# Performance work log

Measured on AMD Instinct MI355X. Metric: run time of the kernel, lower is better.

Reference implementation:

```python
import jax, jax.numpy as jnp
import numpy as np

DEGREE = 5
LN_EPS = 1e-5


def _xavier(key, shape):
    fan_in, fan_out = shape[-1] if len(shape) == 2 else shape[1] * shape[2], shape[0]
    limit = float(np.sqrt(6.0 / (fan_in + fan_out)))
    return jax.random.uniform(key, shape, jnp.float32, -limit, limit)


def setup_inputs() -> dict:
    key = jax.random.key(0)
    ks = jax.random.split(key, 6)
    B, D0, D1, D2 = 16384, 1024, 1024, 512
    return {
        "x": jax.random.normal(ks[0], (B, D0), jnp.float32),
        "coeff1": _xavier(ks[1], (D1, D0, DEGREE + 1)),
        "base_w1": _xavier(ks[2], (D1, D0)),
        "bias1": jnp.zeros((D1,), jnp.float32),
        "ln_gamma": jnp.ones((D1,), jnp.float32),
        "ln_beta": jnp.zeros((D1,), jnp.float32),
        "coeff2": _xavier(ks[3], (D2, D1, DEGREE + 1)),
        "base_w2": _xavier(ks[4], (D2, D1)),
        "bias2": jnp.zeros((D2,), jnp.float32),
    }


def _cheb_layer(x, coeff, base_w, bias):
    # x: [B, I]; coeff: [O, I, D+1]; base_w: [O, I]; bias: [O]
    xn = jnp.tanh(x)
    polys = [jnp.ones_like(xn), xn]
    for _ in range(2, DEGREE + 1):
        polys.append(2.0 * xn * polys[-1] - polys[-2])
    cheb = jnp.stack(polys, axis=-1)  # [B, I, D+1]
    y = jnp.einsum("bid,oid->bo", cheb, coeff)
    y = y + x @ base_w.T + bias
    return y


def _layernorm(h, gamma, beta):
    mu = jnp.mean(h, axis=-1, keepdims=True)
    var = jnp.mean(jnp.square(h - mu), axis=-1, keepdims=True)
    return (h - mu) * jax.lax.rsqrt(var + LN_EPS) * gamma + beta


def reference(x, coeff1, base_w1, bias1, ln_gamma, ln_beta, coeff2, base_w2, bias2):
    x = jnp.tanh(x)  # input_normalization='tanh'
    h = _cheb_layer(x, coeff1, base_w1, bias1)
    h = _layernorm(h, ln_gamma, ln_beta)
    h = h * jax.nn.sigmoid(h)  # SiLU
    out = _cheb_layer(h, coeff2, base_w2, bias2)
    return out
```

## Files before the change

### kernel.cpp

```cpp
#include <hip/hip_runtime.h>


typedef __bf16 bf16x8 __attribute__((ext_vector_type(8)));
typedef float f32x4 __attribute__((ext_vector_type(4)));
typedef unsigned short u16x8 __attribute__((ext_vector_type(8)));

__device__ __forceinline__ unsigned short f2bf(float f) {
    unsigned int u = __float_as_uint(f);
    unsigned int r = (u + 0x7FFFu + ((u >> 16) & 1u)) >> 16;
    return (unsigned short)r;
}
__device__ __forceinline__ float bf2f(unsigned short b) {
    return __uint_as_float(((unsigned int)b) << 16);
}

__device__ __forceinline__ float fast_tanh(float x) {
    float a = fminf(fmaxf(x, -15.f), 15.f);
    float e = __expf(2.f * a);
    return 1.f - 2.f * __builtin_amdgcn_rcpf(e + 1.f);
}
__device__ __forceinline__ float fast_silu(float y) {
    float a = fminf(fmaxf(y, -30.f), 30.f);
    return y * __builtin_amdgcn_rcpf(1.f + __expf(-a));
}

__device__ __forceinline__ void cheb_pack(float s, unsigned short* o6) {
    float u  = fast_tanh(s);
    float T1 = u;
    float T2 = 2.f * u * u - 1.f;
    float T3 = 2.f * u * T2 - T1;
    float T4 = 2.f * u * T3 - T2;
    float T5 = 2.f * u * T4 - T3;
    o6[0] = f2bf(T1); o6[1] = f2bf(T2); o6[2] = f2bf(T3);
    o6[3] = f2bf(T4); o6[4] = f2bf(T5); o6[5] = f2bf(s);
}

__device__ __forceinline__ void load_lds16(const void* g, void* l) {
    __builtin_amdgcn_global_load_lds(
        (const __attribute__((address_space(1))) void*)g,
        (__attribute__((address_space(3))) void*)l, 16, 0, 0);
}

__global__ __launch_bounds__(256) void prep_w_kernel(
    const float* __restrict__ coeff, const float* __restrict__ base_w,
    unsigned short* __restrict__ W, int OI)
{
    int idx = blockIdx.x * 256 + threadIdx.x;
    if (idx >= OI) return;
    const float* c = coeff + (size_t)idx * 6;
    unsigned short w0 = f2bf(c[1]), w1 = f2bf(c[2]), w2 = f2bf(c[3]),
                   w3 = f2bf(c[4]), w4 = f2bf(c[5]), w5 = f2bf(base_w[idx]);
    unsigned int* d = (unsigned int*)(W + (size_t)idx * 6);
    d[0] = w0 | ((unsigned int)w1 << 16);
    d[1] = w2 | ((unsigned int)w3 << 16);
    d[2] = w4 | ((unsigned int)w5 << 16);
}

__global__ __launch_bounds__(256) void prep_bias_kernel(
    const float* __restrict__ coeff, const float* __restrict__ bias,
    float* __restrict__ bp, int I)
{
    int o = blockIdx.x, tid = threadIdx.x;
    float s = 0.f;
    for (int i = tid; i < I; i += 256) s += coeff[((size_t)o * I + i) * 6];
    #pragma unroll
    for (int off = 32; off > 0; off >>= 1) s += __shfl_down(s, off);
    __shared__ float red[4];
    int lane = tid & 63, wv = tid >> 6;
    if (lane == 0) red[wv] = s;
    __syncthreads();
    if (tid == 0) bp[o] = bias[o] + red[0] + red[1] + red[2] + red[3];
}

__global__ __launch_bounds__(256) void expand1_kernel(
    const float* __restrict__ x, unsigned short* __restrict__ Xa)
{
    int b = blockIdx.x, tid = threadIdx.x;
    f32x4 xv = *(const f32x4*)(x + (size_t)b * 1024 + tid * 4);
    alignas(16) unsigned short ov[24];
    #pragma unroll
    for (int e = 0; e < 4; e++) cheb_pack(fast_tanh(xv[e]), ov + e * 6);
    u16x8* dst = (u16x8*)(Xa + (size_t)b * 6144 + tid * 24);
    const u16x8* src = (const u16x8*)ov;
    dst[0] = src[0]; dst[1] = src[1]; dst[2] = src[2];
}

__global__ __launch_bounds__(256) void ln_silu_expand_kernel(
    const unsigned short* __restrict__ H, const float* __restrict__ gamma,
    const float* __restrict__ beta, unsigned short* __restrict__ Xa)
{
    int b = blockIdx.x, tid = threadIdx.x;
    ushort4 hb = *(const ushort4*)(H + (size_t)b * 1024 + tid * 4);
    float hv[4] = { bf2f(hb.x), bf2f(hb.y), bf2f(hb.z), bf2f(hb.w) };
    float s1 = hv[0] + hv[1] + hv[2] + hv[3];
    float s2 = hv[0]*hv[0] + hv[1]*hv[1] + hv[2]*hv[2] + hv[3]*hv[3];
    #pragma unroll
    for (int off = 32; off > 0; off >>= 1) {
        s1 += __shfl_down(s1, off);
        s2 += __shfl_down(s2, off);
    }
    __shared__ float red[8];
    __shared__ float stats[2];
    int lane = tid & 63, wv = tid >> 6;
    if (lane == 0) { red[wv] = s1; red[4 + wv] = s2; }
    __syncthreads();
    if (tid == 0) {
        float t1 = red[0] + red[1] + red[2] + red[3];
        float t2 = red[4] + red[5] + red[6] + red[7];
        float mu = t1 * (1.f / 1024.f);
        float var = t2 * (1.f / 1024.f) - mu * mu;
        stats[0] = mu;
        stats[1] = rsqrtf(var + 1e-5f);
    }
    __syncthreads();
    float mu = stats[0], rs = stats[1];
    f32x4 g  = *(const f32x4*)(gamma + tid * 4);
    f32x4 bt = *(const f32x4*)(beta  + tid * 4);
    alignas(16) unsigned short ov[24];
    #pragma unroll
    for (int e = 0; e < 4; e++) {
        float y = (hv[e] - mu) * rs * g[e] + bt[e];
        cheb_pack(fast_silu(y), ov + e * 6);
    }
    u16x8* dst = (u16x8*)(Xa + (size_t)b * 6144 + tid * 24);
    const u16x8* src = (const u16x8*)ov;
    dst[0] = src[0]; dst[1] = src[1]; dst[2] = src[2];
}

template<int BM, bool OUT_BF16>
__global__ __launch_bounds__(256, 4) void gemm_kernel(
    const unsigned short* __restrict__ A,
    const unsigned short* __restrict__ Wt,
    const float* __restrict__ bias,
    void* __restrict__ Cout,
    int N, int K)
{
    constexpr int MI = BM / 32;
    __shared__ __align__(16) unsigned short As[BM * 64];
    __shared__ __align__(16) unsigned short Bs[128 * 64];
    const int tid  = threadIdx.x;
    const int lane = tid & 63;
    const int wave = tid >> 6;
    const int ntn  = N >> 7;

    int bkid = blockIdx.x;
    const int nm = gridDim.x / ntn;
    int mt, nt;
    if ((nm & 7) == 0) {
        const int mg = nm >> 3;
        const int s  = bkid >> 3;
        const int q  = s / ntn;
        mt = (bkid & 7) * mg + q;
        nt = s - q * ntn;
    } else {
        mt = bkid / ntn; nt = bkid % ntn;
    }
    const size_t m0 = (size_t)mt * BM;
    const size_t n0 = (size_t)nt << 7;

    const int wr = (wave >> 1) * (BM / 2);
    const int wc = (wave & 1) * 64;
    const int fr = lane & 15;
    const int cg = lane >> 4;
    const int srow = tid >> 3;
    const int schunk = (tid & 7) ^ (srow & 7);

    const int fr7 = fr & 7;
    const unsigned short* fA0 = As + (wr + fr) * 64 + ((cg    ) ^ fr7) * 8;
    const unsigned short* fA1 = As + (wr + fr) * 64 + ((cg + 4) ^ fr7) * 8;
    const unsigned short* fB0 = Bs + (wc + fr) * 64 + ((cg    ) ^ fr7) * 8;
    const unsigned short* fB1 = Bs + (wc + fr) * 64 + ((cg + 4) ^ fr7) * 8;

    const unsigned short* Agu = A  + m0 * (size_t)K;
    const unsigned short* Bgu = Wt + n0 * (size_t)K;
    const int loff = srow * K + schunk * 8;

    f32x4 acc[MI][4];
    #pragma unroll
    for (int i = 0; i < MI; i++)
        #pragma unroll
        for (int j = 0; j < 4; j++) acc[i][j] = f32x4{0.f, 0.f, 0.f, 0.f};

    for (int k0 = 0; k0 < K; k0 += 64) {
        const unsigned short* ak = Agu + k0;
        const unsigned short* bk = Bgu + k0;
        #pragma unroll
        for (int s = 0; s < BM / 32; ++s)
            load_lds16(ak + s * 32 * K + loff, &As[(s * 256 + wave * 64) * 8]);
        #pragma unroll
        for (int s = 0; s < 4; ++s)
            load_lds16(bk + s * 32 * K + loff, &Bs[(s * 256 + wave * 64) * 8]);
        __syncthreads();

        bf16x8 af[MI], bfr[4];
        #pragma unroll
        for (int i = 0; i < MI; i++) af[i]  = *(const bf16x8*)(fA0 + i * 1024);
        #pragma unroll
        for (int j = 0; j < 4; j++)  bfr[j] = *(const bf16x8*)(fB0 + j * 1024);
        #pragma unroll
        for (int i = 0; i < MI; i++)
            #pragma unroll
            for (int j = 0; j < 4; j++)
                acc[i][j] = __builtin_amdgcn_mfma_f32_16x16x32_bf16(
                    af[i], bfr[j], acc[i][j], 0, 0, 0);
        #pragma unroll
        for (int i = 0; i < MI; i++) af[i]  = *(const bf16x8*)(fA1 + i * 1024);
        #pragma unroll
        for (int j = 0; j < 4; j++)  bfr[j] = *(const bf16x8*)(fB1 + j * 1024);
        #pragma unroll
        for (int i = 0; i < MI; i++)
            #pragma unroll
            for (int j = 0; j < 4; j++)
                acc[i][j] = __builtin_amdgcn_mfma_f32_16x16x32_bf16(
                    af[i], bfr[j], acc[i][j], 0, 0, 0);
        __syncthreads();
    }

    const int rbase = wr + (lane >> 4) * 4;
    const int cbase = wc + (lane & 15);
    #pragma unroll
    for (int j = 0; j < 4; j++) {
        const int col = (int)n0 + cbase + j * 16;
        const float bv = bias[col];
        #pragma unroll
        for (int i = 0; i < MI; i++) {
            #pragma unroll
            for (int r = 0; r < 4; r++) {
                const size_t idx = (m0 + rbase + i * 16 + r) * N + col;
                if (OUT_BF16)
                    ((unsigned short*)Cout)[idx] = f2bf(acc[i][j][r] + bv);
                else
                    ((float*)Cout)[idx] = acc[i][j][r] + bv;
            }
        }
    }
}

extern "C" void kernel_launch(void* const* d_in, const int* in_sizes, int n_in,
                              void* d_out, int out_size, void* d_ws, size_t ws_size,
                              hipStream_t stream)
{
    const float* x       = (const float*)d_in[0];
    const float* coeff1  = (const float*)d_in[1];
    const float* base_w1 = (const float*)d_in[2];
    const float* bias1   = (const float*)d_in[3];
    const float* gamma   = (const float*)d_in[4];
    const float* beta    = (const float*)d_in[5];
    const float* coeff2  = (const float*)d_in[6];
    const float* base_w2 = (const float*)d_in[7];
    const float* bias2   = (const float*)d_in[8];
    float* out = (float*)d_out;

    const int B = 16384, D0 = 1024, D1 = 1024, D2 = 512;
    const int K1 = D0 * 6, K2 = D1 * 6;

    char* base = (char*)d_ws;
    size_t off = 0;
    unsigned short* W1 = (unsigned short*)(base + off); off += (size_t)D1 * K1 * 2;
    unsigned short* W2 = (unsigned short*)(base + off); off += (size_t)D2 * K2 * 2;
    float* b1p = (float*)(base + off); off += (size_t)D1 * 4;
    float* b2p = (float*)(base + off); off += (size_t)D2 * 4;
    off = (off + 255) & ~(size_t)255;

    size_t per_row = (size_t)K1 * 2 + (size_t)D1 * 2;
    long long avail = (long long)ws_size - (long long)off;
    long long mcl = avail > 0 ? avail / (long long)per_row : 0;
    int Mc = (int)((mcl / 128) * 128);
    if (Mc < 128) Mc = 128;
    if (Mc > B) Mc = B;

    unsigned short* Xa = (unsigned short*)(base + off);
    unsigned short* h = (unsigned short*)(base + off + (size_t)Mc * K1 * 2);

    prep_w_kernel<<<(D1 * D0 + 255) / 256, 256, 0, stream>>>(coeff1, base_w1, W1, D1 * D0);
    prep_w_kernel<<<(D2 * D1 + 255) / 256, 256, 0, stream>>>(coeff2, base_w2, W2, D2 * D1);
    prep_bias_kernel<<<D1, 256, 0, stream>>>(coeff1, bias1, b1p, D0);
    prep_bias_kernel<<<D2, 256, 0, stream>>>(coeff2, bias2, b2p, D1);

    for (int m0 = 0; m0 < B; m0 += Mc) {
        int rows = (B - m0 < Mc) ? (B - m0) : Mc;
        expand1_kernel<<<rows, 256, 0, stream>>>(x + (size_t)m0 * D0, Xa);
        gemm_kernel<128, true><<<(rows / 128) * (D1 / 128), 256, 0, stream>>>(
            Xa, W1, b1p, h, D1, K1);
        ln_silu_expand_kernel<<<rows, 256, 0, stream>>>(h, gamma, beta, Xa);
        gemm_kernel<64, false><<<(rows / 64) * (D2 / 128), 256, 0, stream>>>(
            Xa, W2, b2p, out + (size_t)m0 * D2, D2, K2);
    }
}
```

Before: 627.2 us.

## Replace GEMM with 8-wave 256-row tile, double-buffered LDS ping-pong pipeline

Replaces the single-buffered 4-wave GEMM with an 8-wave kernel that uses 256-row tiles, 256- or 128-column tiles and double-buffered LDS. Global-to-LDS loads for the next K tiles are interleaved between MFMA phases, with explicit vmcnt waits, barriers and s_setprio. The goal is to hide memory latency behind compute and raise arithmetic intensity per tile. The costs are much more LDS per block, lower occupancy (launch bounds of 2 blocks per CU), and a chunk size that must now be a multiple of 256 rows.

```diff
diff --git a/kernel.cpp b/kernel.cpp
--- a/kernel.cpp
+++ b/kernel.cpp
@@ -127,113 +127,191 @@
     dst[0] = src[0]; dst[1] = src[1]; dst[2] = src[2];
 }
 
-template<int BM, bool OUT_BF16>
-__global__ __launch_bounds__(256, 4) void gemm_kernel(
+#define FENCE() asm volatile("" ::: "memory")
+
+#define PH_MID() do { \
+    FENCE(); __builtin_amdgcn_s_barrier(); \
+    asm volatile("s_waitcnt lgkmcnt(0)" ::: "memory"); \
+    __builtin_amdgcn_sched_barrier(0); \
+    __builtin_amdgcn_s_setprio(1); } while (0)
+
+#define PH_END() do { \
+    __builtin_amdgcn_s_setprio(0); \
+    FENCE(); __builtin_amdgcn_s_barrier(); FENCE(); } while (0)
+
+#define VM_STEADY() do { \
+    if constexpr (BN == 256) asm volatile("s_waitcnt vmcnt(8)" ::: "memory"); \
+    else                     asm volatile("s_waitcnt vmcnt(6)" ::: "memory"); } while (0)
+#define VM_DRAIN() asm volatile("s_waitcnt vmcnt(0)" ::: "memory")
+
+#define RD_A(DST0, DST1, BASE, MH) do { \
+    _Pragma("unroll") \
+    for (int mf = 0; mf < 4; ++mf) { \
+        const unsigned short* p_ = (BASE) + ((MH) * 64 + mf * 16) * 64; \
+        DST0[mf] = *(const bf16x8*)(p_ + c0); \
+        DST1[mf] = *(const bf16x8*)(p_ + c1); \
+    } } while (0)
+
+#define RD_B(DST, BASE, CSEL) do { \
+    _Pragma("unroll") \
+    for (int nf = 0; nf < FN; ++nf) \
+        DST[nf] = *(const bf16x8*)((BASE) + (nf * 16) * 64 + (CSEL)); \
+    } while (0)
+
+#define QUAD(MH, AV, BV) do { \
+    _Pragma("unroll") \
+    for (int mf = 0; mf < 4; ++mf) \
+        _Pragma("unroll") \
+        for (int nf = 0; nf < FN; ++nf) \
+            acc[MH][mf][nf] = __builtin_amdgcn_mfma_f32_16x16x32_bf16( \
+                AV[mf], BV[nf], acc[MH][mf][nf], 0, 0, 0); \
+    } while (0)
+
+template<int BN, bool OUT_BF16>
+__global__ __launch_bounds__(512, 2) void gemm8_kernel(
     const unsigned short* __restrict__ A,
     const unsigned short* __restrict__ Wt,
     const float* __restrict__ bias,
     void* __restrict__ Cout,
-    int N, int K)
-{
-    constexpr int MI = BM / 32;
-    __shared__ __align__(16) unsigned short As[BM * 64];
-    __shared__ __align__(16) unsigned short Bs[128 * 64];
+    int N, int K, int NMT)
+{
+    constexpr int FN   = BN / 64;
+    constexpr int BUPW = BN / 64;
+
+    __shared__ __align__(16) unsigned short As[2 * 256 * 64];
+    __shared__ __align__(16) unsigned short Bs[2 * BN * 64];
+
     const int tid  = threadIdx.x;
     const int lane = tid & 63;
     const int wave = tid >> 6;
-    const int ntn  = N >> 7;
-
-    int bkid = blockIdx.x;
-    const int nm = gridDim.x / ntn;
-    int mt, nt;
-    if ((nm & 7) == 0) {
-        const int mg = nm >> 3;
-        const int s  = bkid >> 3;
-        const int q  = s / ntn;
-        mt = (bkid & 7) * mg + q;
-        nt = s - q * ntn;
-    } else {
-        mt = bkid / ntn; nt = bkid % ntn;
-    }
-    const size_t m0 = (size_t)mt * BM;
-    const size_t n0 = (size_t)nt << 7;
-
-    const int wr = (wave >> 1) * (BM / 2);
-    const int wc = (wave & 1) * 64;
-    const int fr = lane & 15;
-    const int cg = lane >> 4;
-    const int srow = tid >> 3;
-    const int schunk = (tid & 7) ^ (srow & 7);
-
+    const int wm   = wave >> 2;
+    const int wn   = wave & 3;
+
+    int wg = blockIdx.x;
+    {
+        const int nwg = gridDim.x;
+        if ((nwg & 7) == 0) {
+            const int cpx = nwg >> 3;
+            wg = (wg & 7) * cpx + (wg >> 3);
+        }
+    }
+    const int mt = wg % NMT;
+    const int nt = wg / NMT;
+    const size_t m0 = (size_t)mt * 256;
+    const size_t n0 = (size_t)nt * BN;
+
+    const int srow   = lane >> 3;
+    const int schunk = (lane & 7) ^ (srow & 7);
+    const unsigned short* Ag = A  + (m0 + srow) * (size_t)K + schunk * 8;
+    const unsigned short* Bg = Wt + (n0 + srow) * (size_t)K + schunk * 8;
+
+    const int fr  = lane & 15;
+    const int cg  = lane >> 4;
     const int fr7 = fr & 7;
-    const unsigned short* fA0 = As + (wr + fr) * 64 + ((cg    ) ^ fr7) * 8;
-    const unsigned short* fA1 = As + (wr + fr) * 64 + ((cg + 4) ^ fr7) * 8;
-    const unsigned short* fB0 = Bs + (wc + fr) * 64 + ((cg    ) ^ fr7) * 8;
-    const unsigned short* fB1 = Bs + (wc + fr) * 64 + ((cg + 4) ^ fr7) * 8;
-
-    const unsigned short* Agu = A  + m0 * (size_t)K;
-    const unsigned short* Bgu = Wt + n0 * (size_t)K;
-    const int loff = srow * K + schunk * 8;
-
-    f32x4 acc[MI][4];
-    #pragma unroll
-    for (int i = 0; i < MI; i++)
+    const int c0  = ((cg    ) ^ fr7) << 3;
+    const int c1  = ((cg + 4) ^ fr7) << 3;
+
+    const int NT = K >> 6;
+
+    const unsigned short* A0f = As + fr * 64 + (wm * 128) * 64;
+    const unsigned short* A1f = A0f + 256 * 64;
+    const unsigned short* B0f = Bs + fr * 64 + (wn * (BN / 4)) * 64;
+    const unsigned short* B1f = B0f + BN * 64;
+
+    auto stageA = [&](int kt, int bsel) {
+        const unsigned short* g = Ag + kt * 64;
+        unsigned short* l = As + bsel * (256 * 64);
         #pragma unroll
-        for (int j = 0; j < 4; j++) acc[i][j] = f32x4{0.f, 0.f, 0.f, 0.f};
-
-    for (int k0 = 0; k0 < K; k0 += 64) {
-        const unsigned short* ak = Agu + k0;
-        const unsigned short* bk = Bgu + k0;
+        for (int j = 0; j < 4; ++j) {
+            const int u = wave * 4 + j;
+            load_lds16(g + (size_t)(u * 8) * K, l + u * 512);
+        }
+    };
+    auto stageB = [&](int kt, int bsel) {
+        const unsigned short* g = Bg + kt * 64;
+        unsigned short* l = Bs + bsel * (BN * 64);
         #pragma unroll
-        for (int s = 0; s < BM / 32; ++s)
-            load_lds16(ak + s * 32 * K + loff, &As[(s * 256 + wave * 64) * 8]);
+        for (int j = 0; j < BUPW; ++j) {
+            const int u = wave * BUPW + j;
+            load_lds16(g + (size_t)(u * 8) * K, l + u * 512);
+        }
+    };
+
+    f32x4 acc[2][4][FN];
+    #pragma unroll
+    for (int mh = 0; mh < 2; ++mh)
         #pragma unroll
-        for (int s = 0; s < 4; ++s)
-            load_lds16(bk + s * 32 * K + loff, &Bs[(s * 256 + wave * 64) * 8]);
-        __syncthreads();
-
-        bf16x8 af[MI], bfr[4];
+        for (int mf = 0; mf < 4; ++mf)
+            #pragma unroll
+            for (int nf = 0; nf < FN; ++nf)
+                acc[mh][mf][nf] = f32x4{0.f, 0.f, 0.f, 0.f};
+
+    stageB(0, 0); stageA(0, 0);
+    stageB(1, 1); stageA(1, 1);
+    VM_STEADY();
+    FENCE(); __builtin_amdgcn_s_barrier(); FENCE();
+
+    for (int kt = 0; kt < NT; kt += 2) {
+        const bool st = (kt + 4) <= NT;
+        bf16x8 a0[4], a1[4], b0[FN], b1[FN];
+
+        RD_A(a0, a1, A0f, 0);
+        RD_B(b0, B0f, c0);
+        PH_MID(); QUAD(0, a0, b0); PH_END();
+
+        RD_B(b1, B0f, c1);
+        PH_MID(); QUAD(0, a1, b1); PH_END();
+
+        RD_A(a0, a1, A0f, 1);
+        if (st) stageB(kt + 2, 0);
+        PH_MID(); QUAD(1, a0, b0); PH_END();
+
+        if (st) { stageA(kt + 2, 0); VM_STEADY(); }
+        else    { VM_DRAIN(); }
+        PH_MID(); QUAD(1, a1, b1); PH_END();
+
+        RD_A(a0, a1, A1f, 0);
+        RD_B(b0, B1f, c0);
+        PH_MID(); QUAD(0, a0, b0); PH_END();
+
+        RD_B(b1, B1f, c1);
+        PH_MID(); QUAD(0, a1, b1); PH_END();
+
+        RD_A(a0, a1, A1f, 1);
+        if (st) stageB(kt + 3, 1);
+        PH_MID(); QUAD(1, a0, b0); PH_END();
+
+        if (st) { stageA(kt + 3, 1); VM_STEADY(); }
+        else    { VM_DRAIN(); }
+        PH_MID(); QUAD(1, a1, b1); PH_END();
+    }
+
+    const size_t rbase0 = m0 + wm * 128 + ((lane >> 4) << 2);
+    const int cb = lane & 15;
+    int colg[FN]; float bv[FN];
+    #pragma unroll
+    for (int nf = 0; nf < FN; ++nf) {
+        colg[nf] = (int)n0 + wn * (BN / 4) + nf * 16 + cb;
+        bv[nf] = bias[colg[nf]];
+    }
+    #pragma unroll
+    for (int mh = 0; mh < 2; ++mh)
         #pragma unroll
-        for (int i = 0; i < MI; i++) af[i]  = *(const bf16x8*)(fA0 + i * 1024);
-        #pragma unroll
-        for (int j = 0; j < 4; j++)  bfr[j] = *(const bf16x8*)(fB0 + j * 1024);
-        #pragma unroll
-        for (int i = 0; i < MI; i++)
+        for (int mf = 0; mf < 4; ++mf) {
+            const size_t rg0 = rbase0 + mh * 64 + mf * 16;
             #pragma unroll
-            for (int j = 0; j < 4; j++)
-                acc[i][j] = __builtin_amdgcn_mfma_f32_16x16x32_bf16(
-                    af[i], bfr[j], acc[i][j], 0, 0, 0);
-        #pragma unroll
-        for (int i = 0; i < MI; i++) af[i]  = *(const bf16x8*)(fA1 + i * 1024);
-        #pragma unroll
-        for (int j = 0; j < 4; j++)  bfr[j] = *(const bf16x8*)(fB1 + j * 1024);
-        #pragma unroll
-        for (int i = 0; i < MI; i++)
-            #pragma unroll
-            for (int j = 0; j < 4; j++)
-                acc[i][j] = __builtin_amdgcn_mfma_f32_16x16x32_bf16(
-                    af[i], bfr[j], acc[i][j], 0, 0, 0);
-        __syncthreads();
-    }
-
-    const int rbase = wr + (lane >> 4) * 4;
-    const int cbase = wc + (lane & 15);
-    #pragma unroll
-    for (int j = 0; j < 4; j++) {
-        const int col = (int)n0 + cbase + j * 16;
-        const float bv = bias[col];
-        #pragma unroll
-        for (int i = 0; i < MI; i++) {
-            #pragma unroll
-            for (int r = 0; r < 4; r++) {
-                const size_t idx = (m0 + rbase + i * 16 + r) * N + col;
-                if (OUT_BF16)
-                    ((unsigned short*)Cout)[idx] = f2bf(acc[i][j][r] + bv);
-                else
-                    ((float*)Cout)[idx] = acc[i][j][r] + bv;
+            for (int r = 0; r < 4; ++r) {
+                const size_t rowoff = (rg0 + r) * (size_t)N;
+                #pragma unroll
+                for (int nf = 0; nf < FN; ++nf) {
+                    const float v = acc[mh][mf][nf][r] + bv[nf];
+                    if constexpr (OUT_BF16)
+                        ((unsigned short*)Cout)[rowoff + colg[nf]] = f2bf(v);
+                    else
+                        ((float*)Cout)[rowoff + colg[nf]] = v;
+                }
             }
         }
-    }
 }
 
 extern "C" void kernel_launch(void* const* d_in, const int* in_sizes, int n_in,
@@ -265,8 +343,8 @@
     size_t per_row = (size_t)K1 * 2 + (size_t)D1 * 2;
     long long avail = (long long)ws_size - (long long)off;
     long long mcl = avail > 0 ? avail / (long long)per_row : 0;
-    int Mc = (int)((mcl / 128) * 128);
-    if (Mc < 128) Mc = 128;
+    int Mc = (int)((mcl / 256) * 256);
+    if (Mc < 256) Mc = 256;
     if (Mc > B) Mc = B;
 
     unsigned short* Xa = (unsigned short*)(base + off);
@@ -279,11 +357,12 @@
 
     for (int m0 = 0; m0 < B; m0 += Mc) {
         int rows = (B - m0 < Mc) ? (B - m0) : Mc;
+        int nmt = rows / 256;
         expand1_kernel<<<rows, 256, 0, stream>>>(x + (size_t)m0 * D0, Xa);
-        gemm_kernel<128, true><<<(rows / 128) * (D1 / 128), 256, 0, stream>>>(
-            Xa, W1, b1p, h, D1, K1);
+        gemm8_kernel<256, true><<<nmt * (D1 / 256), 512, 0, stream>>>(
+            Xa, W1, b1p, h, D1, K1, nmt);
         ln_silu_expand_kernel<<<rows, 256, 0, stream>>>(h, gamma, beta, Xa);
-        gemm_kernel<64, false><<<(rows / 64) * (D2 / 128), 256, 0, stream>>>(
-            Xa, W2, b2p, out + (size_t)m0 * D2, D2, K2);
-    }
-}
+        gemm8_kernel<128, false><<<nmt * (D2 / 128), 512, 0, stream>>>(
+            Xa, W2, b2p, out + (size_t)m0 * D2, D2, K2, nmt);
+    }
+}
```

Result: slower. 678.8 us (+8.2%).

## Add 256x256 eight-wave double-buffered GEMM for first Chebyshev layer

Applied to the files above, without the earlier changes.

Replaces the first-layer GEMM with a new 512-thread kernel that computes 256x256 output tiles. It double-buffers A and B in LDS with direct global-to-LDS loads and uses hand-placed waitcnt, barrier and setprio calls to overlap MFMA work with LDS reads and global prefetch. The larger tile is meant to raise arithmetic intensity and hide memory latency. In exchange it uses far more LDS (128 KB) and registers per block, so occupancy is lower, and the row chunk size is now rounded to 256.

```diff
diff --git a/kernel.cpp b/kernel.cpp
--- a/kernel.cpp
+++ b/kernel.cpp
@@ -127,14 +127,207 @@
     dst[0] = src[0]; dst[1] = src[1]; dst[2] = src[2];
 }
 
-template<int BM, bool OUT_BF16>
+#define FENCE() asm volatile("" ::: "memory")
+#define MIDB()  do { FENCE(); __builtin_amdgcn_s_barrier(); } while (0)
+#define ENDB()  do { __builtin_amdgcn_s_setprio(0); FENCE(); \
+                     __builtin_amdgcn_s_barrier(); FENCE(); } while (0)
+#define LG0() do { asm volatile("s_waitcnt lgkmcnt(0)" ::: "memory"); \
+                   __builtin_amdgcn_sched_barrier(0); } while (0)
+#define LG4() do { asm volatile("s_waitcnt lgkmcnt(4)" ::: "memory"); \
+                   __builtin_amdgcn_sched_barrier(0); } while (0)
+#define LG8() do { asm volatile("s_waitcnt lgkmcnt(8)" ::: "memory"); \
+                   __builtin_amdgcn_sched_barrier(0); } while (0)
+#define VMC0() asm volatile("s_waitcnt vmcnt(0)" ::: "memory")
+#define VMC4() asm volatile("s_waitcnt vmcnt(4)" ::: "memory")
+#define VMC8() asm volatile("s_waitcnt vmcnt(8)" ::: "memory")
+#define SB0()  __builtin_amdgcn_sched_barrier(0)
+
+#define RD_A4(DST, BASE, MH, CS) do { \
+    _Pragma("unroll") \
+    for (int mf = 0; mf < 4; ++mf) \
+        DST[mf] = *(const bf16x8*)((BASE) + ((MH) * 64 + mf * 16) * 64 + (CS)); \
+    } while (0)
+#define RD_B4(DST, BASE, CS) do { \
+    _Pragma("unroll") \
+    for (int nf = 0; nf < 4; ++nf) \
+        DST[nf] = *(const bf16x8*)((BASE) + (nf * 16) * 64 + (CS)); \
+    } while (0)
+
+#define QUAD(MH, AV, BV) do { \
+    __builtin_amdgcn_s_setprio(1); \
+    _Pragma("unroll") \
+    for (int mf = 0; mf < 4; ++mf) \
+        _Pragma("unroll") \
+        for (int nf = 0; nf < 4; ++nf) \
+            acc[MH][mf][nf] = __builtin_amdgcn_mfma_f32_16x16x32_bf16( \
+                AV[mf], BV[nf], acc[MH][mf][nf], 0, 0, 0); \
+    } while (0)
+
+__global__ __launch_bounds__(512, 2) void gemm8_kernel(
+    const unsigned short* __restrict__ A,
+    const unsigned short* __restrict__ Wt,
+    const float* __restrict__ bias,
+    unsigned short* __restrict__ Cout,
+    int N, int K, int NMT)
+{
+    __shared__ __align__(16) unsigned short As[2 * 256 * 64];
+    __shared__ __align__(16) unsigned short Bs[2 * 256 * 64];
+
+    const int tid  = threadIdx.x;
+    const int lane = tid & 63;
+    const int wave = tid >> 6;
+    const int wm   = wave >> 2;
+    const int wn   = wave & 3;
+
+    int wg = blockIdx.x;
+    {
+        const int nwg = gridDim.x;
+        if ((nwg & 7) == 0) {
+            const int cpx = nwg >> 3;
+            wg = (wg & 7) * cpx + (wg >> 3);
+        }
+    }
+    const int mt = wg % NMT;
+    const int nt = wg / NMT;
+    const size_t m0 = (size_t)mt * 256;
+    const size_t n0 = (size_t)nt * 256;
+
+    const int srow   = lane >> 3;
+    const int schunk = (lane & 7) ^ (srow & 7);
+    const unsigned short* Ag = A  + (m0 + srow) * (size_t)K + schunk * 8;
+    const unsigned short* Bg = Wt + (n0 + srow) * (size_t)K + schunk * 8;
+
+    const int fr  = lane & 15;
+    const int cg  = lane >> 4;
+    const int fr7 = fr & 7;
+    const int c0  = ((cg    ) ^ fr7) << 3;
+    const int c1  = ((cg + 4) ^ fr7) << 3;
+
+    const int NT = K >> 6;
+
+    const unsigned short* A0f = As + fr * 64 + (wm * 128) * 64;
+    const unsigned short* A1f = A0f + 256 * 64;
+    const unsigned short* B0f = Bs + fr * 64 + (wn * 64) * 64;
+    const unsigned short* B1f = B0f + 256 * 64;
+
+    auto stageA = [&](int kt, int bsel) {
+        const unsigned short* g = Ag + kt * 64;
+        unsigned short* l = As + bsel * (256 * 64);
+        #pragma unroll
+        for (int j = 0; j < 4; ++j) {
+            const int u = wave * 4 + j;
+            load_lds16(g + (size_t)(u * 8) * K, l + u * 512);
+        }
+    };
+    auto stageB = [&](int kt, int bsel) {
+        const unsigned short* g = Bg + kt * 64;
+        unsigned short* l = Bs + bsel * (256 * 64);
+        #pragma unroll
+        for (int j = 0; j < 4; ++j) {
+            const int u = wave * 4 + j;
+            load_lds16(g + (size_t)(u * 8) * K, l + u * 512);
+        }
+    };
+
+    f32x4 acc[2][4][4];
+    #pragma unroll
+    for (int mh = 0; mh < 2; ++mh)
+        #pragma unroll
+        for (int mf = 0; mf < 4; ++mf)
+            #pragma unroll
+            for (int nf = 0; nf < 4; ++nf)
+                acc[mh][mf][nf] = f32x4{0.f, 0.f, 0.f, 0.f};
+
+    bf16x8 aP[4], aQ[4], b0[4], b1[4];
+
+    stageB(0, 0); stageA(0, 0); stageB(1, 1);
+    VMC4();
+    MIDB(); FENCE();
+    RD_B4(b0, B0f, c0);
+    SB0();
+
+    for (int kt = 0; kt < NT; kt += 2) {
+        const bool st = (kt + 4) <= NT;
+
+        RD_A4(aP, A0f, 0, c0);
+        SB0();
+        RD_A4(aQ, A0f, 0, c1);
+        RD_B4(b1, B0f, c1);
+        stageA(kt + 1, 1);
+        MIDB(); LG8();
+        QUAD(0, aP, b0); ENDB();
+
+        RD_A4(aP, A0f, 1, c0);
+        MIDB(); LG4();
+        QUAD(0, aQ, b1); ENDB();
+
+        RD_A4(aQ, A0f, 1, c1);
+        if (st) { stageB(kt + 2, 0); VMC8(); }
+        else    { VMC4(); }
+        MIDB(); LG4();
+        QUAD(1, aP, b0); ENDB();
+
+        RD_B4(b0, B1f, c0);
+        if (st) VMC4(); else VMC0();
+        MIDB(); LG4();
+        QUAD(1, aQ, b1); ENDB();
+
+        RD_A4(aP, A1f, 0, c0);
+        SB0();
+        RD_A4(aQ, A1f, 0, c1);
+        RD_B4(b1, B1f, c1);
+        if (st) stageA(kt + 2, 0);
+        MIDB(); LG8();
+        QUAD(0, aP, b0); ENDB();
+
+        RD_A4(aP, A1f, 1, c0);
+        MIDB(); LG4();
+        QUAD(0, aQ, b1); ENDB();
+
+        RD_A4(aQ, A1f, 1, c1);
+        if (st) { stageB(kt + 3, 1); VMC8(); }
+        else    { VMC0(); }
+        MIDB(); LG4();
+        QUAD(1, aP, b0); ENDB();
+
+        if (st) { RD_B4(b0, B0f, c0); SB0(); VMC4(); }
+        else    { VMC0(); }
+        MIDB();
+        if (st) { LG4(); } else { LG0(); }
+        QUAD(1, aQ, b1); ENDB();
+    }
+
+    const size_t rbase0 = m0 + wm * 128 + ((lane >> 4) << 2);
+    const int cb = lane & 15;
+    int colg[4]; float bv[4];
+    #pragma unroll
+    for (int nf = 0; nf < 4; ++nf) {
+        colg[nf] = (int)n0 + wn * 64 + nf * 16 + cb;
+        bv[nf] = bias[colg[nf]];
+    }
+    #pragma unroll
+    for (int mh = 0; mh < 2; ++mh)
+        #pragma unroll
+        for (int mf = 0; mf < 4; ++mf) {
+            const size_t rg0 = rbase0 + mh * 64 + mf * 16;
+            #pragma unroll
+            for (int r = 0; r < 4; ++r) {
+                const size_t rowoff = (rg0 + r) * (size_t)N;
+                #pragma unroll
+                for (int nf = 0; nf < 4; ++nf)
+                    Cout[rowoff + colg[nf]] = f2bf(acc[mh][mf][nf][r] + bv[nf]);
+            }
+        }
+}
+
 __global__ __launch_bounds__(256, 4) void gemm_kernel(
     const unsigned short* __restrict__ A,
     const unsigned short* __restrict__ Wt,
     const float* __restrict__ bias,
-    void* __restrict__ Cout,
+    float* __restrict__ Cout,
     int N, int K)
 {
+    constexpr int BM = 64;
     constexpr int MI = BM / 32;
     __shared__ __align__(16) unsigned short As[BM * 64];
     __shared__ __align__(16) unsigned short Bs[128 * 64];
@@ -227,10 +420,7 @@
             #pragma unroll
             for (int r = 0; r < 4; r++) {
                 const size_t idx = (m0 + rbase + i * 16 + r) * N + col;
-                if (OUT_BF16)
-                    ((unsigned short*)Cout)[idx] = f2bf(acc[i][j][r] + bv);
-                else
-                    ((float*)Cout)[idx] = acc[i][j][r] + bv;
+                Cout[idx] = acc[i][j][r] + bv;
             }
         }
     }
@@ -265,8 +455,8 @@
     size_t per_row = (size_t)K1 * 2 + (size_t)D1 * 2;
     long long avail = (long long)ws_size - (long long)off;
     long long mcl = avail > 0 ? avail / (long long)per_row : 0;
-    int Mc = (int)((mcl / 128) * 128);
-    if (Mc < 128) Mc = 128;
+    int Mc = (int)((mcl / 256) * 256);
+    if (Mc < 256) Mc = 256;
     if (Mc > B) Mc = B;
 
     unsigned short* Xa = (unsigned short*)(base + off);
@@ -279,11 +469,12 @@
 
     for (int m0 = 0; m0 < B; m0 += Mc) {
         int rows = (B - m0 < Mc) ? (B - m0) : Mc;
+        int nmt = rows / 256;
         expand1_kernel<<<rows, 256, 0, stream>>>(x + (size_t)m0 * D0, Xa);
-        gemm_kernel<128, true><<<(rows / 128) * (D1 / 128), 256, 0, stream>>>(
-            Xa, W1, b1p, h, D1, K1);
+        gemm8_kernel<<<nmt * (D1 / 256), 512, 0, stream>>>(
+            Xa, W1, b1p, h, D1, K1, nmt);
         ln_silu_expand_kernel<<<rows, 256, 0, stream>>>(h, gamma, beta, Xa);
-        gemm_kernel<64, false><<<(rows / 64) * (D2 / 128), 256, 0, stream>>>(
+        gemm_kernel<<<(rows / 64) * (D2 / 128), 256, 0, stream>>>(
             Xa, W2, b2p, out + (size_t)m0 * D2, D2, K2);
     }
 }
```

After: 699.7 us. 11.6% more time.

## Add triple-buffered 256x128 GEMM kernel for first Chebyshev layer

Applied to the files above, without the earlier changes.

Replaces the first layer's GEMM with a new kernel that uses 256x128 tiles, a three-stage LDS ring filled by direct global-to-LDS loads with an XOR swizzle, and register double-buffered fragments interleaved with MFMA issue under raised wave priority. The aim is to hide global and LDS latency behind matrix math and raise arithmetic intensity per tile. The second GEMM keeps the old kernel, now specialised to fp32 output. It uses more LDS and registers (occupancy 2), and the row chunk size now rounds to 256.

```diff
diff --git a/kernel.cpp b/kernel.cpp
--- a/kernel.cpp
+++ b/kernel.cpp
@@ -127,14 +127,171 @@
     dst[0] = src[0]; dst[1] = src[1]; dst[2] = src[2];
 }
 
-template<int BM, bool OUT_BF16>
+__global__ __launch_bounds__(256, 2) void gemm5_kernel(
+    const unsigned short* __restrict__ A,
+    const unsigned short* __restrict__ Wt,
+    const float* __restrict__ bias,
+    unsigned short* __restrict__ Cout,
+    int N, int K, int NMT)
+{
+    constexpr int ASZ = 256 * 32;
+    constexpr int BSZ = 128 * 32;
+    __shared__ __align__(16) unsigned short As[3 * ASZ];
+    __shared__ __align__(16) unsigned short Bs[3 * BSZ];
+
+    const int tid  = threadIdx.x;
+    const int lane = tid & 63;
+    const int wave = tid >> 6;
+    const int wm   = wave >> 1;
+    const int wn   = wave & 1;
+
+    int wg = blockIdx.x;
+    {
+        const int nwg = gridDim.x;
+        if ((nwg & 7) == 0) { const int cpx = nwg >> 3; wg = (wg & 7) * cpx + (wg >> 3); }
+    }
+    const int mt = wg % NMT;
+    const int nt = wg / NMT;
+    const size_t m0 = (size_t)mt * 256;
+    const size_t n0 = (size_t)nt * 128;
+
+    const int cs   = (((lane & 3) ^ ((lane >> 3) & 3)) << 3);
+    const int srow = lane >> 2;
+    const unsigned short* AgJ[4];
+    unsigned short* AD[4];
+    #pragma unroll
+    for (int j = 0; j < 4; ++j) {
+        const int u = wave * 4 + j;
+        AgJ[j] = A + (m0 + (size_t)(u * 16 + srow)) * K + cs;
+        AD[j]  = As + u * 512 + lane * 8;
+    }
+    const unsigned short* BgJ[2];
+    unsigned short* BD[2];
+    #pragma unroll
+    for (int j = 0; j < 2; ++j) {
+        const int u = wave * 2 + j;
+        BgJ[j] = Wt + (n0 + (size_t)(u * 16 + srow)) * K + cs;
+        BD[j]  = Bs + u * 512 + lane * 8;
+    }
+
+    const int fr = lane & 15;
+    const int cg = lane >> 4;
+    const int ck = ((cg ^ ((fr >> 1) & 3)) << 3);
+    const unsigned short* PA = As + (wm * 128 + fr) * 32 + ck;
+    const unsigned short* PB = Bs + (wn * 64 + fr) * 32 + ck;
+
+    const int NT = K >> 5;
+
+    f32x4 acc[2][4][4];
+    #pragma unroll
+    for (int mh = 0; mh < 2; ++mh)
+        #pragma unroll
+        for (int mf = 0; mf < 4; ++mf)
+            #pragma unroll
+            for (int nf = 0; nf < 4; ++nf)
+                acc[mh][mf][nf] = f32x4{0.f, 0.f, 0.f, 0.f};
+
+    bf16x8 aF[8], aG[8], bF[4], bG[4];
+
+#define STAGE(T, R_) do { \
+    const size_t ko_ = (size_t)(T) * 32; \
+    load_lds16(AgJ[0] + ko_, AD[0] + (R_) * ASZ); \
+    load_lds16(AgJ[1] + ko_, AD[1] + (R_) * ASZ); \
+    load_lds16(AgJ[2] + ko_, AD[2] + (R_) * ASZ); \
+    load_lds16(AgJ[3] + ko_, AD[3] + (R_) * ASZ); \
+    load_lds16(BgJ[0] + ko_, BD[0] + (R_) * BSZ); \
+    load_lds16(BgJ[1] + ko_, BD[1] + (R_) * BSZ); \
+} while (0)
+
+#define RD(AF_, BF_, R_) do { \
+    _Pragma("unroll") \
+    for (int mh = 0; mh < 2; ++mh) \
+        _Pragma("unroll") \
+        for (int mf = 0; mf < 4; ++mf) \
+            AF_[mh * 4 + mf] = *(const bf16x8*)(PA + (R_) * ASZ + (mh * 64 + mf * 16) * 32); \
+    _Pragma("unroll") \
+    for (int nf = 0; nf < 4; ++nf) \
+        BF_[nf] = *(const bf16x8*)(PB + (R_) * BSZ + nf * 16 * 32); \
+} while (0)
+
+#define MM(AF_, BF_) do { \
+    __builtin_amdgcn_s_setprio(1); \
+    _Pragma("unroll") \
+    for (int mh = 0; mh < 2; ++mh) \
+        _Pragma("unroll") \
+        for (int mf = 0; mf < 4; ++mf) \
+            _Pragma("unroll") \
+            for (int nf = 0; nf < 4; ++nf) \
+                acc[mh][mf][nf] = __builtin_amdgcn_mfma_f32_16x16x32_bf16( \
+                    AF_[mh * 4 + mf], BF_[nf], acc[mh][mf][nf], 0, 0, 0); \
+    __builtin_amdgcn_s_setprio(0); \
+} while (0)
+
+#define W6() do { \
+    asm volatile("s_waitcnt vmcnt(6) lgkmcnt(0)" ::: "memory"); \
+    __builtin_amdgcn_s_barrier(); } while (0)
+#define W0() do { \
+    asm volatile("s_waitcnt vmcnt(0) lgkmcnt(0)" ::: "memory"); \
+    __builtin_amdgcn_s_barrier(); } while (0)
+
+    STAGE(0, 0); STAGE(1, 1); STAGE(2, 2);
+    asm volatile("s_waitcnt vmcnt(12)" ::: "memory");
+    __builtin_amdgcn_s_barrier();
+    RD(aF, bF, 0);
+
+    for (int t = 0; t < NT - 8; t += 6) {
+        W6(); RD(aG, bG, 1); STAGE(t + 3, 0); MM(aF, bF);
+        W6(); RD(aF, bF, 2); STAGE(t + 4, 1); MM(aG, bG);
+        W6(); RD(aG, bG, 0); STAGE(t + 5, 2); MM(aF, bF);
+        W6(); RD(aF, bF, 1); STAGE(t + 6, 0); MM(aG, bG);
+        W6(); RD(aG, bG, 2); STAGE(t + 7, 1); MM(aF, bF);
+        W6(); RD(aF, bF, 0); STAGE(t + 8, 2); MM(aG, bG);
+    }
+    W6(); RD(aG, bG, 1); STAGE(NT - 3, 0); MM(aF, bF);
+    W6(); RD(aF, bF, 2); STAGE(NT - 2, 1); MM(aG, bG);
+    W6(); RD(aG, bG, 0); STAGE(NT - 1, 2); MM(aF, bF);
+    W6(); RD(aF, bF, 1); MM(aG, bG);
+    W0(); RD(aG, bG, 2); MM(aF, bF);
+    asm volatile("s_waitcnt lgkmcnt(0)" ::: "memory");
+    MM(aG, bG);
+
+#undef STAGE
+#undef RD
+#undef MM
+#undef W6
+#undef W0
+
+    const size_t rbase0 = m0 + wm * 128 + ((lane >> 4) << 2);
+    const int cb = lane & 15;
+    int colg[4]; float bv[4];
+    #pragma unroll
+    for (int nf = 0; nf < 4; ++nf) {
+        colg[nf] = (int)n0 + wn * 64 + nf * 16 + cb;
+        bv[nf] = bias[colg[nf]];
+    }
+    #pragma unroll
+    for (int mh = 0; mh < 2; ++mh)
+        #pragma unroll
+        for (int mf = 0; mf < 4; ++mf) {
+            const size_t rg0 = rbase0 + mh * 64 + mf * 16;
+            #pragma unroll
+            for (int r = 0; r < 4; ++r) {
+                const size_t rowoff = (rg0 + r) * (size_t)N;
+                #pragma unroll
+                for (int nf = 0; nf < 4; ++nf)
+                    Cout[rowoff + colg[nf]] = f2bf(acc[mh][mf][nf][r] + bv[nf]);
+            }
+        }
+}
+
 __global__ __launch_bounds__(256, 4) void gemm_kernel(
     const unsigned short* __restrict__ A,
     const unsigned short* __restrict__ Wt,
     const float* __restrict__ bias,
-    void* __restrict__ Cout,
+    float* __restrict__ Cout,
     int N, int K)
 {
+    constexpr int BM = 64;
     constexpr int MI = BM / 32;
     __shared__ __align__(16) unsigned short As[BM * 64];
     __shared__ __align__(16) unsigned short Bs[128 * 64];
@@ -227,10 +384,7 @@
             #pragma unroll
             for (int r = 0; r < 4; r++) {
                 const size_t idx = (m0 + rbase + i * 16 + r) * N + col;
-                if (OUT_BF16)
-                    ((unsigned short*)Cout)[idx] = f2bf(acc[i][j][r] + bv);
-                else
-                    ((float*)Cout)[idx] = acc[i][j][r] + bv;
+                Cout[idx] = acc[i][j][r] + bv;
             }
         }
     }
@@ -265,8 +419,8 @@
     size_t per_row = (size_t)K1 * 2 + (size_t)D1 * 2;
     long long avail = (long long)ws_size - (long long)off;
     long long mcl = avail > 0 ? avail / (long long)per_row : 0;
-    int Mc = (int)((mcl / 128) * 128);
-    if (Mc < 128) Mc = 128;
+    int Mc = (int)((mcl / 256) * 256);
+    if (Mc < 256) Mc = 256;
     if (Mc > B) Mc = B;
 
     unsigned short* Xa = (unsigned short*)(base + off);
@@ -279,11 +433,12 @@
 
     for (int m0 = 0; m0 < B; m0 += Mc) {
         int rows = (B - m0 < Mc) ? (B - m0) : Mc;
+        int nmt = rows / 256;
         expand1_kernel<<<rows, 256, 0, stream>>>(x + (size_t)m0 * D0, Xa);
-        gemm_kernel<128, true><<<(rows / 128) * (D1 / 128), 256, 0, stream>>>(
-            Xa, W1, b1p, h, D1, K1);
+        gemm5_kernel<<<nmt * (D1 / 128), 256, 0, stream>>>(
+            Xa, W1, b1p, h, D1, K1, nmt);
         ln_silu_expand_kernel<<<rows, 256, 0, stream>>>(h, gamma, beta, Xa);
-        gemm_kernel<64, false><<<(rows / 64) * (D2 / 128), 256, 0, stream>>>(
+        gemm_kernel<<<(rows / 64) * (D2 / 128), 256, 0, stream>>>(
             Xa, W2, b2p, out + (size_t)m0 * D2, D2, K2);
     }
 }
```

Result: slower. 761.4 us (+21.4%).
